# Kernel tuning notes

Measured on AMD Instinct MI355X. Metric: run time of the kernel, lower is better.

The kernel has to match this reference:

```python
import jax, jax.numpy as jnp
import numpy as np

K = 2  # top-k experts per token


def setup_inputs() -> dict:
    key = jax.random.key(0)
    k1, k2 = jax.random.split(key)
    B, S, H, E = 4, 4096, 4096, 64
    x = jax.random.normal(k1, (B, S, H), dtype=jnp.float32)
    gate_w = jax.random.normal(k2, (E, H), dtype=jnp.float32) * (H ** -0.5)
    return {"x": x, "gate_w": gate_w}


def reference(x, gate_w):
    # logits = x @ gate_w.T : [B, S, E]
    logits = jnp.einsum("bsh,eh->bse", x, gate_w)
    scores = jax.nn.softmax(logits, axis=-1)
    topk_scores, topk_idx = jax.lax.top_k(scores, K)  # [B, S, K]
    aux_loss = scores.mean() * 0.0
    z_loss = jnp.mean(logits.astype(jnp.float32) ** 2)
    return topk_idx, topk_scores, aux_loss, z_loss
```

## Files before the change

kernel.cpp:

```cpp
#include <hip/hip_runtime.h>
#include <hip/hip_bf16.h>


typedef __bf16  bf16x8  __attribute__((ext_vector_type(8)));
typedef float   f32x16  __attribute__((ext_vector_type(16)));

#define BS_TOK 16384
#define H_DIM  4096
#define E_DIM  64
#define KSPLIT 4
#define KCHUNK (H_DIM / KSPLIT)
#define WS_ZBUF_OFF (1536u << 10)
#define WS_LG_OFF   (2u << 20)

__device__ __forceinline__ void split3(float v, __bf16 &b0, __bf16 &b1, __bf16 &b2) {
    b0 = (__bf16)v;
    float r = v - (float)b0;
    b1 = (__bf16)r;
    float r2 = r - (float)b1;
    b2 = (__bf16)r2;
}

__global__ void prep_w(const float* __restrict__ gw, bf16x8* __restrict__ wb) {
    int idx  = blockIdx.x * blockDim.x + threadIdx.x;
    int kb   = idx >> 7;
    int rem  = idx & 127;
    int nt   = rem >> 6;
    int lane = rem & 63;
    int n  = nt * 32 + (lane & 31);
    int kk = kb * 16 + ((lane >> 5) << 3);
    const float* p = gw + (size_t)n * H_DIM + kk;
    bf16x8 t0, t1, t2;
#pragma unroll
    for (int j = 0; j < 8; ++j) {
        __bf16 a, b, c;
        split3(p[j], a, b, c);
        t0[j] = a; t1[j] = b; t2[j] = c;
    }
    size_t fb = (size_t)(kb * 2 + nt) * 3;
    wb[(fb + 0) * 64 + lane] = t0;
    wb[(fb + 1) * 64 + lane] = t1;
    wb[(fb + 2) * 64 + lane] = t2;
}

__global__ __launch_bounds__(256, 4) void gemm_split(
        const float* __restrict__ x, const bf16x8* __restrict__ wb,
        float* __restrict__ lg) {
    __shared__ float red[64 * 64];

    int bid = blockIdx.x;
    int mt  = bid >> 2;
    int kc  = bid & 3;
    int tid = threadIdx.x;
    int w   = tid >> 6;
    int l   = tid & 63;
    int m0  = mt * 64;
    int rw  = (w & 1) * 32;
    int kh  = w >> 1;

    int row  = rw + (l & 31);
    int half = l >> 5;

    const float4* gp = (const float4*)(x + (size_t)(m0 + row) * H_DIM
                                         + (size_t)(kc * KCHUNK + kh * 512 + half * 8));
    const bf16x8* wp = wb + (size_t)(kc * 64 + kh * 32) * (6 * 64) + l;

    f32x16 acc0, acc1;
#pragma unroll
    for (int r = 0; r < 16; ++r) { acc0[r] = 0.f; acc1[r] = 0.f; }

    float4 pa = gp[0];
    float4 pb = gp[1];

#pragma unroll 2
    for (int ks = 0; ks < 32; ++ks) {
        float4 ca = pa, cb = pb;
        int nk = (ks + 1) & 31;
        pa = gp[nk * 4];
        pb = gp[nk * 4 + 1];

        bf16x8 a0, a1, a2;
        float xs[8] = {ca.x, ca.y, ca.z, ca.w, cb.x, cb.y, cb.z, cb.w};
#pragma unroll
        for (int j = 0; j < 8; ++j) {
            __bf16 h0, h1, h2;
            split3(xs[j], h0, h1, h2);
            a0[j] = h0; a1[j] = h1; a2[j] = h2;
        }

        const bf16x8* wq = wp + (size_t)ks * (6 * 64);
        bf16x8 b0 = wq[0 * 64], b1 = wq[1 * 64], b2 = wq[2 * 64];
        bf16x8 b3 = wq[3 * 64], b4 = wq[4 * 64], b5 = wq[5 * 64];

        acc0 = __builtin_amdgcn_mfma_f32_32x32x16_bf16(a0, b0, acc0, 0, 0, 0);
        acc0 = __builtin_amdgcn_mfma_f32_32x32x16_bf16(a1, b0, acc0, 0, 0, 0);
        acc0 = __builtin_amdgcn_mfma_f32_32x32x16_bf16(a2, b0, acc0, 0, 0, 0);
        acc0 = __builtin_amdgcn_mfma_f32_32x32x16_bf16(a0, b1, acc0, 0, 0, 0);
        acc0 = __builtin_amdgcn_mfma_f32_32x32x16_bf16(a1, b1, acc0, 0, 0, 0);
        acc0 = __builtin_amdgcn_mfma_f32_32x32x16_bf16(a0, b2, acc0, 0, 0, 0);
        acc1 = __builtin_amdgcn_mfma_f32_32x32x16_bf16(a0, b3, acc1, 0, 0, 0);
        acc1 = __builtin_amdgcn_mfma_f32_32x32x16_bf16(a1, b3, acc1, 0, 0, 0);
        acc1 = __builtin_amdgcn_mfma_f32_32x32x16_bf16(a2, b3, acc1, 0, 0, 0);
        acc1 = __builtin_amdgcn_mfma_f32_32x32x16_bf16(a0, b4, acc1, 0, 0, 0);
        acc1 = __builtin_amdgcn_mfma_f32_32x32x16_bf16(a1, b4, acc1, 0, 0, 0);
        acc1 = __builtin_amdgcn_mfma_f32_32x32x16_bf16(a0, b5, acc1, 0, 0, 0);
    }

    int col = l & 31;
    if (kh == 1) {
#pragma unroll
        for (int r = 0; r < 16; ++r) {
            int mm = rw + (r & 3) + ((r >> 2) << 3) + (half << 2);
            red[mm * 64 + col]      = acc0[r];
            red[mm * 64 + 32 + col] = acc1[r];
        }
    }
    __syncthreads();
    if (kh == 0) {
        size_t obase = (size_t)kc * BS_TOK * E_DIM + (size_t)m0 * E_DIM;
#pragma unroll
        for (int r = 0; r < 16; ++r) {
            int mm = rw + (r & 3) + ((r >> 2) << 3) + (half << 2);
            lg[obase + (size_t)mm * E_DIM + col]
                = acc0[r] + red[mm * 64 + col];
            lg[obase + (size_t)mm * E_DIM + 32 + col]
                = acc1[r] + red[mm * 64 + 32 + col];
        }
    }
}

__global__ __launch_bounds__(256) void epilogue(const float* __restrict__ lg,
                                                float* __restrict__ out,
                                                float* __restrict__ zbuf) {
    __shared__ float zsh[4];
    int lane = threadIdx.x & 63;
    int w    = threadIdx.x >> 6;
    int t    = blockIdx.x * 4 + w;

    float l = 0.f;
#pragma unroll
    for (int s = 0; s < KSPLIT; ++s)
        l += lg[((size_t)s * BS_TOK + t) * E_DIM + lane];

    float z = l * l;
#pragma unroll
    for (int off = 32; off; off >>= 1) z += __shfl_xor(z, off);
    if (lane == 0) zsh[w] = z;

    float m = l;
#pragma unroll
    for (int off = 32; off; off >>= 1) m = fmaxf(m, __shfl_xor(m, off));
    float e = expf(l - m);
    float d = e;
#pragma unroll
    for (int off = 32; off; off >>= 1) d += __shfl_xor(d, off);
    float sc = e / d;

    float s1 = sc; int i1 = lane;
#pragma unroll
    for (int off = 32; off; off >>= 1) {
        float os = __shfl_xor(s1, off); int oi = __shfl_xor(i1, off);
        if (os > s1 || (os == s1 && oi < i1)) { s1 = os; i1 = oi; }
    }
    float sm = (lane == i1) ? -1.0f : sc;
    float s2 = sm; int i2 = lane;
#pragma unroll
    for (int off = 32; off; off >>= 1) {
        float os = __shfl_xor(s2, off); int oi = __shfl_xor(i2, off);
        if (os > s2 || (os == s2 && oi < i2)) { s2 = os; i2 = oi; }
    }

    if (lane == 0) {
        out[2 * t]                  = (float)i1;
        out[2 * t + 1]              = (float)i2;
        out[2 * BS_TOK + 2 * t]     = s1;
        out[2 * BS_TOK + 2 * t + 1] = s2;
    }
    __syncthreads();
    if (threadIdx.x == 0)
        zbuf[blockIdx.x] = zsh[0] + zsh[1] + zsh[2] + zsh[3];
}

__global__ __launch_bounds__(256) void zreduce(const float* __restrict__ zbuf,
                                               float* __restrict__ out) {
    __shared__ float sh[4];
    int tid = threadIdx.x;
    float s = 0.f;
#pragma unroll
    for (int i = 0; i < 16; ++i) s += zbuf[tid + 256 * i];
#pragma unroll
    for (int off = 32; off; off >>= 1) s += __shfl_xor(s, off);
    if ((tid & 63) == 0) sh[tid >> 6] = s;
    __syncthreads();
    if (tid == 0) {
        out[4 * BS_TOK]     = 0.0f;
        out[4 * BS_TOK + 1] = (sh[0] + sh[1] + sh[2] + sh[3])
                              * (1.0f / (float)(BS_TOK * E_DIM));
    }
}

extern "C" void kernel_launch(void* const* d_in, const int* in_sizes, int n_in,
                              void* d_out, int out_size, void* d_ws, size_t ws_size,
                              hipStream_t stream) {
    const float* x  = (const float*)d_in[0];
    const float* gw = (const float*)d_in[1];
    float* out  = (float*)d_out;
    bf16x8* wb  = (bf16x8*)d_ws;
    float*  zbf = (float*)((char*)d_ws + WS_ZBUF_OFF);
    float*  lg  = (float*)((char*)d_ws + WS_LG_OFF);

    prep_w<<<128, 256, 0, stream>>>(gw, wb);
    gemm_split<<<(BS_TOK / 64) * KSPLIT, 256, 0, stream>>>(x, wb, lg);
    epilogue<<<BS_TOK / 4, 256, 0, stream>>>(lg, out, zbf);
    zreduce<<<1, 256, 0, stream>>>(zbf, out);
}
```

Measured before the change: 416.3 us.

## Fuse gating GEMM with softmax/top-k epilogue using async LDS triple-buffering

Replaces the split-K GEMM, its logits round-trip through global memory, and the separate epilogue kernel with a single kernel. Each 512-thread block owns 64 tokens across the full hidden dimension, loads x and the pre-split bf16 weights into LDS with global_load_lds through a three-stage pipeline, reduces the four K-partials in LDS, and then does softmax, top-2 and z-loss in place. This removes the intermediate logits traffic and one launch. In exchange only 256 blocks are launched, which may underfill the GPU, and the loop depends on manual vmcnt waits and barriers.

```diff
diff --git a/kernel.cpp b/kernel.cpp
--- a/kernel.cpp
+++ b/kernel.cpp
@@ -8,10 +8,11 @@
 #define BS_TOK 16384
 #define H_DIM  4096
 #define E_DIM  64
-#define KSPLIT 4
-#define KCHUNK (H_DIM / KSPLIT)
+#define NPAN   64
 #define WS_ZBUF_OFF (1536u << 10)
-#define WS_LG_OFF   (2u << 20)
+
+#define XSLOT(s)  ((s) * 4096)
+#define WSLOT(s)  (12288 + (s) * 6144)
 
 __device__ __forceinline__ void split3(float v, __bf16 &b0, __bf16 &b1, __bf16 &b2) {
     b0 = (__bf16)v;
@@ -19,6 +20,12 @@
     b1 = (__bf16)r;
     float r2 = r - (float)b1;
     b2 = (__bf16)r2;
+}
+
+__device__ __forceinline__ void async_copy16(const float* gp, float* lp) {
+    __builtin_amdgcn_global_load_lds(
+        (const __attribute__((address_space(1))) void*)gp,
+        (__attribute__((address_space(3))) void*)lp, 16, 0, 0);
 }
 
 __global__ void prep_w(const float* __restrict__ gw, bf16x8* __restrict__ wb) {
@@ -43,55 +50,65 @@
     wb[(fb + 2) * 64 + lane] = t2;
 }
 
-__global__ __launch_bounds__(256, 4) void gemm_split(
-        const float* __restrict__ x, const bf16x8* __restrict__ wb,
-        float* __restrict__ lg) {
-    __shared__ float red[64 * 64];
+__global__ __launch_bounds__(512, 2) void fused(
+        const float* __restrict__ x, const float* __restrict__ wbf,
+        float* __restrict__ out, float* __restrict__ zbuf) {
+    __shared__ float lds[30720];
+    __shared__ float zsh[8];
 
     int bid = blockIdx.x;
-    int mt  = bid >> 2;
-    int kc  = bid & 3;
+    int m0  = bid * 64;
     int tid = threadIdx.x;
     int w   = tid >> 6;
     int l   = tid & 63;
-    int m0  = mt * 64;
-    int rw  = (w & 1) * 32;
-    int kh  = w >> 1;
-
-    int row  = rw + (l & 31);
+    int kb  = w & 3;
+    int rh  = w >> 2;
+
+    int row  = rh * 32 + (l & 31);
     int half = l >> 5;
-
-    const float4* gp = (const float4*)(x + (size_t)(m0 + row) * H_DIM
-                                         + (size_t)(kc * KCHUNK + kh * 512 + half * 8));
-    const bf16x8* wp = wb + (size_t)(kc * 64 + kh * 32) * (6 * 64) + l;
+    int rsw  = row & 15;
+    int c0   = kb * 4 + half * 2;
+
+    const float* gx[2]; int xo[2];
+#pragma unroll
+    for (int r = 0; r < 2; ++r) {
+        int g = r * 32 + (tid >> 4);
+        int c = (tid & 15) ^ (g & 15);
+        gx[r] = x + (size_t)(m0 + g) * H_DIM + c * 4;
+        xo[r] = r * 2048 + w * 256;
+    }
+    const float* gwp = wbf + tid * 4;
+    int wo = w * 256;
 
     f32x16 acc0, acc1;
 #pragma unroll
     for (int r = 0; r < 16; ++r) { acc0[r] = 0.f; acc1[r] = 0.f; }
 
-    float4 pa = gp[0];
-    float4 pb = gp[1];
-
-#pragma unroll 2
-    for (int ks = 0; ks < 32; ++ks) {
-        float4 ca = pa, cb = pb;
-        int nk = (ks + 1) & 31;
-        pa = gp[nk * 4];
-        pb = gp[nk * 4 + 1];
-
+    auto stage = [&](int p, int s) {
+#pragma unroll
+        for (int r = 0; r < 2; ++r)
+            async_copy16(gx[r] + p * 64, &lds[XSLOT(s) + xo[r]]);
+#pragma unroll
+        for (int r = 0; r < 3; ++r)
+            async_copy16(gwp + p * 6144 + r * 2048, &lds[WSLOT(s) + r * 2048 + wo]);
+    };
+
+    auto compute = [&](int p, int s) {
+        const float* xb = &lds[XSLOT(s)];
+        float4 xa = *(const float4*)&xb[row * 64 + ((c0 ^ rsw) << 2)];
+        float4 xc = *(const float4*)&xb[row * 64 + (((c0 + 1) ^ rsw) << 2)];
         bf16x8 a0, a1, a2;
-        float xs[8] = {ca.x, ca.y, ca.z, ca.w, cb.x, cb.y, cb.z, cb.w};
+        float xs[8] = {xa.x, xa.y, xa.z, xa.w, xc.x, xc.y, xc.z, xc.w};
 #pragma unroll
         for (int j = 0; j < 8; ++j) {
             __bf16 h0, h1, h2;
             split3(xs[j], h0, h1, h2);
             a0[j] = h0; a1[j] = h1; a2[j] = h2;
         }
-
-        const bf16x8* wq = wp + (size_t)ks * (6 * 64);
-        bf16x8 b0 = wq[0 * 64], b1 = wq[1 * 64], b2 = wq[2 * 64];
-        bf16x8 b3 = wq[3 * 64], b4 = wq[4 * 64], b5 = wq[5 * 64];
-
+        const bf16x8* wl = (const bf16x8*)&lds[WSLOT(s)];
+        int fb = kb * 6 * 64 + l;
+        bf16x8 b0 = wl[fb + 0*64], b1 = wl[fb + 1*64], b2 = wl[fb + 2*64];
+        bf16x8 b3 = wl[fb + 3*64], b4 = wl[fb + 4*64], b5 = wl[fb + 5*64];
         acc0 = __builtin_amdgcn_mfma_f32_32x32x16_bf16(a0, b0, acc0, 0, 0, 0);
         acc0 = __builtin_amdgcn_mfma_f32_32x32x16_bf16(a1, b0, acc0, 0, 0, 0);
         acc0 = __builtin_amdgcn_mfma_f32_32x32x16_bf16(a2, b0, acc0, 0, 0, 0);
@@ -104,90 +121,108 @@
         acc1 = __builtin_amdgcn_mfma_f32_32x32x16_bf16(a0, b4, acc1, 0, 0, 0);
         acc1 = __builtin_amdgcn_mfma_f32_32x32x16_bf16(a1, b4, acc1, 0, 0, 0);
         acc1 = __builtin_amdgcn_mfma_f32_32x32x16_bf16(a0, b5, acc1, 0, 0, 0);
-    }
+    };
+
+    stage(0, 0); stage(1, 1); stage(2, 2);
+
+    int sl = 0;
+#pragma unroll 1
+    for (int p = 0; p < 61; ++p) {
+        asm volatile("s_waitcnt vmcnt(10)" ::: "memory");
+        __builtin_amdgcn_s_barrier();
+        compute(p, sl);
+        __builtin_amdgcn_s_barrier();
+        stage(p + 3, sl);
+        sl = (sl == 2) ? 0 : sl + 1;
+    }
+    asm volatile("s_waitcnt vmcnt(10)" ::: "memory");
+    __builtin_amdgcn_s_barrier();
+    compute(61, 1);
+    asm volatile("s_waitcnt vmcnt(5)" ::: "memory");
+    __builtin_amdgcn_s_barrier();
+    compute(62, 2);
+    asm volatile("s_waitcnt vmcnt(0)" ::: "memory");
+    __builtin_amdgcn_s_barrier();
+    compute(63, 0);
+    __syncthreads();
 
     int col = l & 31;
-    if (kh == 1) {
+    if (kb != 0) {
+        float* b = &lds[kb * 4096];
 #pragma unroll
         for (int r = 0; r < 16; ++r) {
-            int mm = rw + (r & 3) + ((r >> 2) << 3) + (half << 2);
-            red[mm * 64 + col]      = acc0[r];
-            red[mm * 64 + 32 + col] = acc1[r];
-        }
-    }
-    __syncthreads();
-    if (kh == 0) {
-        size_t obase = (size_t)kc * BS_TOK * E_DIM + (size_t)m0 * E_DIM;
+            int mm = rh * 32 + (r & 3) + ((r >> 2) << 3) + (half << 2);
+            b[mm * 64 + col]      = acc0[r];
+            b[mm * 64 + 32 + col] = acc1[r];
+        }
+    }
+    __syncthreads();
+    if (kb == 0) {
 #pragma unroll
         for (int r = 0; r < 16; ++r) {
-            int mm = rw + (r & 3) + ((r >> 2) << 3) + (half << 2);
-            lg[obase + (size_t)mm * E_DIM + col]
-                = acc0[r] + red[mm * 64 + col];
-            lg[obase + (size_t)mm * E_DIM + 32 + col]
-                = acc1[r] + red[mm * 64 + 32 + col];
-        }
-    }
-}
-
-__global__ __launch_bounds__(256) void epilogue(const float* __restrict__ lg,
-                                                float* __restrict__ out,
-                                                float* __restrict__ zbuf) {
-    __shared__ float zsh[4];
-    int lane = threadIdx.x & 63;
-    int w    = threadIdx.x >> 6;
-    int t    = blockIdx.x * 4 + w;
-
-    float l = 0.f;
-#pragma unroll
-    for (int s = 0; s < KSPLIT; ++s)
-        l += lg[((size_t)s * BS_TOK + t) * E_DIM + lane];
-
-    float z = l * l;
-#pragma unroll
-    for (int off = 32; off; off >>= 1) z += __shfl_xor(z, off);
-    if (lane == 0) zsh[w] = z;
-
-    float m = l;
-#pragma unroll
-    for (int off = 32; off; off >>= 1) m = fmaxf(m, __shfl_xor(m, off));
-    float e = expf(l - m);
-    float d = e;
-#pragma unroll
-    for (int off = 32; off; off >>= 1) d += __shfl_xor(d, off);
-    float sc = e / d;
-
-    float s1 = sc; int i1 = lane;
-#pragma unroll
-    for (int off = 32; off; off >>= 1) {
-        float os = __shfl_xor(s1, off); int oi = __shfl_xor(i1, off);
-        if (os > s1 || (os == s1 && oi < i1)) { s1 = os; i1 = oi; }
-    }
-    float sm = (lane == i1) ? -1.0f : sc;
-    float s2 = sm; int i2 = lane;
-#pragma unroll
-    for (int off = 32; off; off >>= 1) {
-        float os = __shfl_xor(s2, off); int oi = __shfl_xor(i2, off);
-        if (os > s2 || (os == s2 && oi < i2)) { s2 = os; i2 = oi; }
-    }
-
-    if (lane == 0) {
-        out[2 * t]                  = (float)i1;
-        out[2 * t + 1]              = (float)i2;
-        out[2 * BS_TOK + 2 * t]     = s1;
-        out[2 * BS_TOK + 2 * t + 1] = s2;
-    }
-    __syncthreads();
-    if (threadIdx.x == 0)
-        zbuf[blockIdx.x] = zsh[0] + zsh[1] + zsh[2] + zsh[3];
+            int mm = rh * 32 + (r & 3) + ((r >> 2) << 3) + (half << 2);
+            int i0 = mm * 64 + col;
+            lds[i0]      = acc0[r] + lds[4096 + i0] + lds[8192 + i0] + lds[12288 + i0];
+            lds[i0 + 32] = acc1[r] + lds[4096 + i0 + 32] + lds[8192 + i0 + 32]
+                                   + lds[12288 + i0 + 32];
+        }
+    }
+    __syncthreads();
+
+    float zacc = 0.f;
+#pragma unroll 1
+    for (int i = 0; i < 8; ++i) {
+        int tl = w * 8 + i;
+        float lv = lds[tl * 64 + l];
+        zacc += lv * lv;
+
+        float m = lv;
+#pragma unroll
+        for (int off = 32; off; off >>= 1) m = fmaxf(m, __shfl_xor(m, off));
+        float e = expf(lv - m);
+        float d = e;
+#pragma unroll
+        for (int off = 32; off; off >>= 1) d += __shfl_xor(d, off);
+        float sc = e / d;
+
+        float s1 = sc; int i1 = l;
+#pragma unroll
+        for (int off = 32; off; off >>= 1) {
+            float os = __shfl_xor(s1, off); int oi = __shfl_xor(i1, off);
+            if (os > s1 || (os == s1 && oi < i1)) { s1 = os; i1 = oi; }
+        }
+        float sm = (l == i1) ? -1.0f : sc;
+        float s2 = sm; int i2 = l;
+#pragma unroll
+        for (int off = 32; off; off >>= 1) {
+            float os = __shfl_xor(s2, off); int oi = __shfl_xor(i2, off);
+            if (os > s2 || (os == s2 && oi < i2)) { s2 = os; i2 = oi; }
+        }
+        if (l == 0) {
+            int t = m0 + tl;
+            out[2 * t]                  = (float)i1;
+            out[2 * t + 1]              = (float)i2;
+            out[2 * BS_TOK + 2 * t]     = s1;
+            out[2 * BS_TOK + 2 * t + 1] = s2;
+        }
+    }
+#pragma unroll
+    for (int off = 32; off; off >>= 1) zacc += __shfl_xor(zacc, off);
+    if (l == 0) zsh[w] = zacc;
+    __syncthreads();
+    if (tid == 0) {
+        float s = 0.f;
+#pragma unroll
+        for (int i = 0; i < 8; ++i) s += zsh[i];
+        zbuf[bid] = s;
+    }
 }
 
 __global__ __launch_bounds__(256) void zreduce(const float* __restrict__ zbuf,
                                                float* __restrict__ out) {
     __shared__ float sh[4];
     int tid = threadIdx.x;
-    float s = 0.f;
-#pragma unroll
-    for (int i = 0; i < 16; ++i) s += zbuf[tid + 256 * i];
+    float s = zbuf[tid];
 #pragma unroll
     for (int off = 32; off; off >>= 1) s += __shfl_xor(s, off);
     if ((tid & 63) == 0) sh[tid >> 6] = s;
@@ -207,10 +242,8 @@
     float* out  = (float*)d_out;
     bf16x8* wb  = (bf16x8*)d_ws;
     float*  zbf = (float*)((char*)d_ws + WS_ZBUF_OFF);
-    float*  lg  = (float*)((char*)d_ws + WS_LG_OFF);
 
     prep_w<<<128, 256, 0, stream>>>(gw, wb);
-    gemm_split<<<(BS_TOK / 64) * KSPLIT, 256, 0, stream>>>(x, wb, lg);
-    epilogue<<<BS_TOK / 4, 256, 0, stream>>>(lg, out, zbf);
+    fused<<<256, 512, 0, stream>>>(x, (const float*)wb, out, zbf);
     zreduce<<<1, 256, 0, stream>>>(zbf, out);
 }
```

Result: no change. 411.7 us (-1.1%).
